# Performance work log

Measured on AMD Instinct MI355X. Metric: run time of the kernel, lower is better.

The kernel has to match this reference:

```python
import jax, jax.numpy as jnp
import numpy as np
from jax import lax

# pywt 'db6' rec_lo (scaling filter). dec_lo = rec_lo[::-1]; pytorch_wavelets
# stores dec filters flipped for conv (=correlation), so analysis correlation
# filters are exactly rec_lo and rec_hi = qmf(rec_lo). Synthesis filters for
# conv_transpose are rec_lo/rec_hi unflipped -> same arrays.
_DB6 = np.array([0.11154074335008017, 0.4946238903983854, 0.7511339080215775,
                 0.3152503517092432, -0.22626469396516913, -0.12976686756709563,
                 0.09750160558707936, 0.02752286553001629, -0.031582039318031156,
                 0.0005538422009938016, 0.004777257511010651, -0.00107730108499558],
                dtype=np.float32)
_QMF = (_DB6[::-1].copy() * ((-1.0) ** np.arange(12))).astype(np.float32)
H0, H1 = jnp.asarray(_DB6), jnp.asarray(_QMF)
LF, J = 12, 3
BATCH, SEQ_LEN, CH = 128, 720, 321
COMP_L = [99, 365, 188, 99]   # [yl, yh1, yh2, yh3] for seq_len=720
OUT_L = [22, 57, 34, 22]      # same decomposition of red_len=104


def afb1d(x):
    """One-level analysis filter bank, mode='symmetric'. x: [B,C,N]."""
    B, C, N = x.shape
    out = (N + LF - 1) // 2                      # pywt dwt_coeff_len (symmetric)
    p = 2 * (out - 1) - N + LF
    xp = jnp.pad(x, ((0, 0), (0, 0), (p // 2, (p + 1) // 2)), mode='symmetric')
    w = jnp.stack([H0, H1])[:, None, :]          # [2,1,LF]
    y = lax.conv_general_dilated(xp.reshape(B * C, 1, -1), w, (2,), 'VALID',
                                 dimension_numbers=('NCH', 'OIH', 'NCH'))
    y = y.reshape(B, C, 2, out)
    return y[:, :, 0], y[:, :, 1]


def sfb1d(lo, hi):
    """One-level synthesis bank == conv_transpose1d(stride=2, padding=LF-2)."""
    B, C, Lin = lo.shape
    z = jnp.stack([lo, hi], axis=2).reshape(B * C, 2, Lin)
    w = jnp.stack([H0[::-1], H1[::-1]])[None]    # [1,2,LF], flipped for corr
    y = lax.conv_general_dilated(z, w, (1,), ((1, 1),), lhs_dilation=(2,),
                                 dimension_numbers=('NCH', 'OIH', 'NCH'))
    return y.reshape(B, C, -1)                   # length 2*Lin + 2 - LF


def sinusoidal_pe(n_pos, d):
    pos = jnp.arange(n_pos, dtype=jnp.float32)[:, None]
    div = jnp.exp(jnp.arange(0, d, 2, dtype=jnp.float32) * (-np.log(10000.0) / d))
    pe = jnp.zeros((n_pos, d), jnp.float32)
    pe = pe.at[:, 0::2].set(jnp.sin(pos * div))
    pe = pe.at[:, 1::2].set(jnp.cos(pos * div[: d // 2]))
    return pe


def _forward(x, qws, qbs, kws, kbs, pws, pbs, iws, als, bes):
    mean = lax.stop_gradient(jnp.mean(x, axis=1, keepdims=True))
    std = lax.stop_gradient(jnp.sqrt(jnp.var(x, axis=1, keepdims=True) + 1e-5))
    xc = jnp.transpose((x - mean) / std, (0, 2, 1))      # [B,C,L]
    yl, yh = xc, []
    for _ in range(J):
        yl, hi = afb1d(yl)
        yh.append(hi)
    decomps = [yl] + yh                                  # lengths COMP_L
    preds = []
    for i, comp in enumerate(decomps):
        B, C, L = comp.shape
        Q = jnp.tanh(comp @ qws[i].T + qbs[i])           # [B,C,L]
        K = jnp.tanh(comp @ kws[i].T + kbs[i])
        scores = jnp.einsum('bcl,bcs->bls', Q, K) / (L ** 0.5)
        weighted = jnp.mean(jnp.tanh(scores), axis=1)    # [B,S] (equal per channel)
        cum = jnp.flip(jnp.cumsum(jnp.flip(weighted, -1), -1), -1)
        P = jax.nn.softmax(cum * als[i][0], axis=-1)
        idxs = jnp.arange(L, dtype=jnp.float32)
        win = jnp.sum(P * idxs, axis=-1)[:, None, None]  # soft truncation [B,1,1]
        mask = jax.nn.sigmoid((idxs[None, None, :] - win) * bes[i][0])
        pred = (comp * mask) @ pws[i].T + pbs[i]         # [B,C,O]
        pred = jax.nn.softmax(iws[i], axis=1) * (pred + sinusoidal_pe(C, pred.shape[-1])[None])
        preds.append(pred)
    ll = preds[0]
    for h in preds[:0:-1]:                               # coarsest high band first
        if ll.shape[-1] > h.shape[-1]:
            ll = ll[..., : h.shape[-1]]
        ll = sfb1d(ll, h)
    return ll, mean, std


def setup_inputs() -> dict:
    key = jax.random.key(0)
    ks = jax.random.split(key, 64)
    inp = {'x': jax.random.normal(ks[0], (BATCH, SEQ_LEN, CH), jnp.float32)}
    k = 1
    for i, (L, O) in enumerate(zip(COMP_L, OUT_L)):
        s = 1.0 / np.sqrt(L)                             # torch Linear default init
        inp[f'qw{i}'] = jax.random.uniform(ks[k], (L, L), jnp.float32, -s, s); k += 1
        inp[f'qb{i}'] = jax.random.uniform(ks[k], (L,), jnp.float32, -s, s); k += 1
        inp[f'kw{i}'] = jax.random.uniform(ks[k], (L, L), jnp.float32, -s, s); k += 1
        inp[f'kb{i}'] = jax.random.uniform(ks[k], (L,), jnp.float32, -s, s); k += 1
        inp[f'pw{i}'] = jnp.full((O, L), 1.0 / L, jnp.float32)
        inp[f'pb{i}'] = jnp.zeros((O,), jnp.float32)
        inp[f'iw{i}'] = jnp.ones((1, CH, O), jnp.float32)
        inp[f'al{i}'] = jnp.full((1,), 10.0, jnp.float32)
        inp[f'be{i}'] = jnp.full((1,), 10.0, jnp.float32)
    return inp


def reference(x, qw0, qb0, kw0, kb0, pw0, pb0, iw0, al0, be0,
              qw1, qb1, kw1, kb1, pw1, pb1, iw1, al1, be1,
              qw2, qb2, kw2, kb2, pw2, pb2, iw2, al2, be2,
              qw3, qb3, kw3, kb3, pw3, pb3, iw3, al3, be3):
    return _forward(x, [qw0, qw1, qw2, qw3], [qb0, qb1, qb2, qb3],
                    [kw0, kw1, kw2, kw3], [kb0, kb1, kb2, kb3],
                    [pw0, pw1, pw2, pw3], [pb0, pb1, pb2, pb3],
                    [iw0, iw1, iw2, iw3], [al0, al1, al2, al3],
                    [be0, be1, be2, be3])
```

## Files before the change

kernel.cpp:

```cpp
#include <hip/hip_runtime.h>
#include <hip/hip_bf16.h>
#include <math.h>

namespace {
constexpr int kB  = 128;
constexpr int kC  = 321;
constexpr int kN0 = 720;
constexpr int kCp = 384;
}

typedef __attribute__((ext_vector_type(8))) short short8;
typedef __attribute__((ext_vector_type(4))) float floatx4;

__constant__ float c_h0[12] = {
  0.11154074335008017f, 0.4946238903983854f, 0.7511339080215775f,
  0.3152503517092432f, -0.22626469396516913f, -0.12976686756709563f,
  0.09750160558707936f, 0.02752286553001629f, -0.031582039318031156f,
  0.0005538422009938016f, 0.004777257511010651f, -0.00107730108499558f};
__constant__ float c_h1[12] = {
  -0.00107730108499558f, -0.004777257511010651f, 0.0005538422009938016f,
  0.031582039318031156f, 0.02752286553001629f, -0.09750160558707936f,
  -0.12976686756709563f, 0.22626469396516913f, 0.3152503517092432f,
  -0.7511339080215775f, 0.4946238903983854f, -0.11154074335008017f};
__constant__ float c_h0r[12] = {
  -0.00107730108499558f, 0.004777257511010651f, 0.0005538422009938016f,
  -0.031582039318031156f, 0.02752286553001629f, 0.09750160558707936f,
  -0.12976686756709563f, -0.22626469396516913f, 0.3152503517092432f,
  0.7511339080215775f, 0.4946238903983854f, 0.11154074335008017f};
__constant__ float c_h1r[12] = {
  -0.11154074335008017f, 0.4946238903983854f, -0.7511339080215775f,
  0.3152503517092432f, 0.22626469396516913f, -0.12976686756709563f,
  -0.09750160558707936f, 0.02752286553001629f, 0.031582039318031156f,
  0.0005538422009938016f, -0.004777257511010651f, -0.00107730108499558f};

__device__ __forceinline__ float fast_tanh(float x) {
  float e = __expf(2.f * x);
  return 1.f - 2.f / (e + 1.f);
}
__device__ __forceinline__ unsigned short f2b(float f) {
  __hip_bfloat16 h = __float2bfloat16(f);
  return __builtin_bit_cast(unsigned short, h);
}

__device__ __forceinline__ void gload16(const unsigned short* g, short* l) {
  __builtin_amdgcn_global_load_lds(
      (const __attribute__((address_space(1))) unsigned int*)g,
      (__attribute__((address_space(3))) unsigned int*)l, 16, 0, 0);
}

__global__ void __launch_bounds__(128) partial_ms_kernel(
    const float* __restrict__ x, float* __restrict__ ps, float* __restrict__ ps2) {
  int b = blockIdx.x, chunk = blockIdx.y;
  int c = blockIdx.z * 128 + threadIdx.x;
  if (c >= kC) return;
  const float* xb = x + (size_t)b * kN0 * kC + c;
  int t0 = chunk * 90;
  float s = 0.f, s2 = 0.f;
#pragma unroll 15
  for (int i = 0; i < 90; ++i) {
    float v = xb[(size_t)(t0 + i) * kC];
    s += v; s2 += v * v;
  }
  ps [(b * 8 + chunk) * kC + c] = s;
  ps2[(b * 8 + chunk) * kC + c] = s2;
}

__global__ void __launch_bounds__(256) finalize_ms_kernel(
    const float* __restrict__ ps, const float* __restrict__ ps2,
    float* __restrict__ mout, float* __restrict__ sout,
    float* __restrict__ meanw, float* __restrict__ invw) {
  int i = blockIdx.x * 256 + threadIdx.x;
  if (i >= kB * kC) return;
  int b = i / kC, c = i - b * kC;
  float s = 0.f, s2 = 0.f;
#pragma unroll
  for (int k = 0; k < 8; ++k) { s += ps[(b * 8 + k) * kC + c]; s2 += ps2[(b * 8 + k) * kC + c]; }
  float mean = s * (1.f / (float)kN0);
  float var = s2 * (1.f / (float)kN0) - mean * mean;
  float sd = sqrtf(var + 1e-5f);
  mout[i] = mean; sout[i] = sd;
  meanw[i] = mean; invw[i] = 1.f / sd;
}

__device__ __forceinline__ int sym_reflect(int t, int N) {
  t = (t < 0) ? (-1 - t) : t;
  t = (t >= N) ? (2 * N - 1 - t) : t;
  return t;
}

template <bool NORM, bool LO_F32, bool LO_BF16>
__global__ void __launch_bounds__(256) dwt_fused_kernel(
    const float* __restrict__ in, const float* __restrict__ meanw,
    const float* __restrict__ invw, float* __restrict__ loF,
    unsigned short* __restrict__ loB, unsigned short* __restrict__ hiB,
    int N, int L, int Lp) {
  __shared__ float xs[138][64];
  __shared__ unsigned short los[64][72];
  __shared__ unsigned short his[64][72];
  const int b = blockIdx.z;
  const int n0 = blockIdx.x * 64, c0 = blockIdx.y * 64;
  const int tid = threadIdx.x;
  const int cl = tid & 63, wv = tid >> 6;
  const int c = c0 + cl;
  const int t0 = 2 * n0 - 10;
  const float* ib = in + (size_t)b * N * kC;
  float mean = 0.f, inv = 1.f;
  if (NORM && c < kC) { mean = meanw[b * kC + c]; inv = invw[b * kC + c]; }
  for (int r = wv; r < 138; r += 4) {
    int t = sym_reflect(t0 + r, N);
    float v = (c < kC) ? ib[(size_t)t * kC + c] : 0.f;
    if (NORM) v = (v - mean) * inv;
    xs[r][cl] = v;
  }
  __syncthreads();
#pragma unroll 4
  for (int k = 0; k < 16; ++k) {
    int nl = wv + 4 * k;
    int n = n0 + nl;
    float a0 = 0.f, a1 = 0.f;
    int base = 2 * nl;
#pragma unroll
    for (int j = 0; j < 12; ++j) {
      float v = xs[base + j][cl];
      a0 += v * c_h0[j]; a1 += v * c_h1[j];
    }
    bool valid = (n < L) && (c < kC);
    if (LO_F32 && valid) loF[((size_t)b * L + n) * kC + c] = a0;
    if (LO_BF16) los[cl][nl] = f2b(valid ? a0 : 0.f);
    his[cl][nl] = f2b(valid ? a1 : 0.f);
  }
  __syncthreads();
  int row = tid >> 2, part = tid & 3;
  size_t dst = ((size_t)b * kCp + c0 + row) * Lp + n0 + part * 16;
  *(uint4*)(hiB + dst)     = *(const uint4*)&his[row][part * 16];
  *(uint4*)(hiB + dst + 8) = *(const uint4*)&his[row][part * 16 + 8];
  if (LO_BF16) {
    *(uint4*)(loB + dst)     = *(const uint4*)&los[row][part * 16];
    *(uint4*)(loB + dst + 8) = *(const uint4*)&los[row][part * 16 + 8];
  }
}

struct WcArgs { const float* src[8]; unsigned short* dst[8]; int L[8]; int Lp[8]; };
__global__ void __launch_bounds__(256) wconv_all_kernel(WcArgs a) {
  int lvl = blockIdx.y;
  int Lp = a.Lp[lvl], L = a.L[lvl];
  int i = blockIdx.x * 256 + threadIdx.x;
  if (i >= Lp * Lp) return;
  int p = i / Lp, l = i - p * Lp;
  a.dst[lvl][i] = f2b((p < L && l < L) ? a.src[lvl][(size_t)p * L + l] : 0.f);
}

struct QKAllArgs {
  const unsigned short* W[8];
  const unsigned short* Xt[4];
  const float* bias[8];
  unsigned short* Y[8];
  int Lp[4], L[4], yOff[4];
};
__global__ void __launch_bounds__(256) qk_all_kernel(QKAllArgs a) {
  const int y = blockIdx.y;
  const int lvl = (y >= a.yOff[1]) + (y >= a.yOff[2]) + (y >= a.yOff[3]);
  const int Lp = a.Lp[lvl], L = a.L[lvl];
  const int pBase = (y - a.yOff[lvl]) * 128;
  const unsigned short* W0 = a.W[2 * lvl]     + (size_t)pBase * Lp;
  const unsigned short* W1 = a.W[2 * lvl + 1] + (size_t)pBase * Lp;
  const int b = blockIdx.z;
  const int cBase = blockIdx.x * 128;
  const int tid = threadIdx.x;
  const int ln = tid & 63, w = tid >> 6;
  const int wm = w & 1, wn = w >> 1;
  __shared__ short Aq[128 * 64];
  __shared__ short Ak[128 * 64];
  __shared__ short Bs[128 * 64];
  floatx4 acc[2][4][4] = {};
  const unsigned short* Xb = a.Xt[lvl] + ((size_t)b * kCp + cBase) * Lp;
  const int kIters = Lp >> 6;
  const int srow = w * 32;
  const int lrow = ln >> 3, lslot = ln & 7;
  const int gswz = (lslot ^ lrow) << 3;
  const int sc0 = (((ln >> 4) + 0) ^ (ln & 7)) << 3;
  const int sc1 = (((ln >> 4) + 4) ^ (ln & 7)) << 3;
  for (int kt = 0; kt < kIters; ++kt) {
    const int lc = kt << 6;
#pragma unroll
    for (int q = 0; q < 4; ++q) {
      const int row = srow + 8 * q + lrow;
      const size_t goff = (size_t)row * Lp + lc + gswz;
      short* ldst = (short*)&Aq[(srow + 8 * q) * 64];
      gload16(W0 + goff, ldst);
      gload16(W1 + goff, ldst + 128 * 64);
      gload16(Xb + goff, ldst + 2 * 128 * 64);
    }
    __syncthreads();
#pragma unroll
    for (int sub = 0; sub < 2; ++sub) {
      const int sc = sub ? sc1 : sc0;
      short8 a0[4], a1[4], bv[4];
#pragma unroll
      for (int mi = 0; mi < 4; ++mi) {
        const int ar = (wm * 64 + mi * 16 + (ln & 15)) * 64 + sc;
        a0[mi] = *(const short8*)&Aq[ar];
        a1[mi] = *(const short8*)&Ak[ar];
      }
#pragma unroll
      for (int ni = 0; ni < 4; ++ni)
        bv[ni] = *(const short8*)&Bs[(wn * 64 + ni * 16 + (ln & 15)) * 64 + sc];
#pragma unroll
      for (int mi = 0; mi < 4; ++mi)
#pragma unroll
        for (int ni = 0; ni < 4; ++ni) {
          acc[0][mi][ni] = __builtin_amdgcn_mfma_f32_16x16x32_bf16(a0[mi], bv[ni], acc[0][mi][ni], 0, 0, 0);
          acc[1][mi][ni] = __builtin_amdgcn_mfma_f32_16x16x32_bf16(a1[mi], bv[ni], acc[1][mi][ni], 0, 0, 0);
        }
    }
    __syncthreads();
  }
#pragma unroll
  for (int s = 0; s < 2; ++s) {
    const float* bias = a.bias[2 * lvl + s];
    unsigned short* Yd = a.Y[2 * lvl + s];
#pragma unroll
    for (int mi = 0; mi < 4; ++mi) {
#pragma unroll
      for (int r = 0; r < 4; ++r) {
        int p = pBase + wm * 64 + mi * 16 + (ln >> 4) * 4 + r;
        float bv = (p < L) ? bias[p] : 0.f;
#pragma unroll
        for (int ni = 0; ni < 4; ++ni) {
          int c = cBase + wn * 64 + ni * 16 + (ln & 15);
          float v = (p < L && c < kC) ? fast_tanh(acc[s][mi][ni][r] + bv) : 0.f;
          Yd[((size_t)b * Lp + p) * kCp + c] = f2b(v);
        }
      }
    }
  }
}

struct ScAllArgs {
  const unsigned short* Q[4]; const unsigned short* K[4];
  float* wgt[4];
  int Lp[4], L[4], tOff[4];
  float scale[4];
};
__global__ void __launch_bounds__(256) scores_all_kernel(ScAllArgs a) {
  const int t = blockIdx.x;
  const int lvl = (t >= a.tOff[1]) + (t >= a.tOff[2]) + (t >= a.tOff[3]);
  const int rel = t - a.tOff[lvl];
  const int Lp = a.Lp[lvl], L = a.L[lvl];
  const int pt = Lp >> 7;
  const int sBase = (rel % pt) * 128;
  const int lBase = (rel / pt) * 128;
  const int b = blockIdx.y;
  const int tid = threadIdx.x;
  const int ln = tid & 63, w = tid >> 6;
  const int wm = w & 1, wn = w >> 1;
  __shared__ short As[128 * 64];
  __shared__ short Bs[128 * 64];
  __shared__ float red[128];
  floatx4 acc[4][4] = {};
  const unsigned short* Qp = a.Q[lvl] + ((size_t)b * Lp + lBase) * kCp;
  const unsigned short* Kp = a.K[lvl] + ((size_t)b * Lp + sBase) * kCp;
  const int srow = w * 32;
  const int lrow = ln >> 3, lslot = ln & 7;
  const int gswz = (lslot ^ lrow) << 3;
  const int sc0 = (((ln >> 4) + 0) ^ (ln & 7)) << 3;
  const int sc1 = (((ln >> 4) + 4) ^ (ln & 7)) << 3;
  for (int cc = 0; cc < kCp; cc += 64) {
#pragma unroll
    for (int q = 0; q < 4; ++q) {
      const int row = srow + 8 * q + lrow;
      const size_t goff = (size_t)row * kCp + cc + gswz;
      short* ldst = (short*)&As[(srow + 8 * q) * 64];
      gload16(Qp + goff, ldst);
      gload16(Kp + goff, ldst + 128 * 64);
    }
    __syncthreads();
#pragma unroll
    for (int sub = 0; sub < 2; ++sub) {
      const int sc = sub ? sc1 : sc0;
      short8 av[4], bv[4];
#pragma unroll
      for (int mi = 0; mi < 4; ++mi)
        av[mi] = *(const short8*)&As[(wm * 64 + mi * 16 + (ln & 15)) * 64 + sc];
#pragma unroll
      for (int ni = 0; ni < 4; ++ni)
        bv[ni] = *(const short8*)&Bs[(wn * 64 + ni * 16 + (ln & 15)) * 64 + sc];
#pragma unroll
      for (int mi = 0; mi < 4; ++mi)
#pragma unroll
        for (int ni = 0; ni < 4; ++ni)
          acc[mi][ni] = __builtin_amdgcn_mfma_f32_16x16x32_bf16(av[mi], bv[ni], acc[mi][ni], 0, 0, 0);
    }
    __syncthreads();
  }
  if (tid < 128) red[tid] = 0.f;
  __syncthreads();
  const float scale = a.scale[lvl];
#pragma unroll
  for (int ni = 0; ni < 4; ++ni) {
    float p = 0.f;
#pragma unroll
    for (int mi = 0; mi < 4; ++mi)
#pragma unroll
      for (int r = 0; r < 4; ++r) p += fast_tanh(acc[mi][ni][r] * scale);
    p += __shfl_xor(p, 16);
    p += __shfl_xor(p, 32);
    if ((ln & 48) == 0) atomicAdd(&red[wn * 64 + ni * 16 + (ln & 15)], p);
  }
  __syncthreads();
  if (tid < 128) {
    int s = sBase + tid;
    if (s < L) atomicAdd(&a.wgt[lvl][(size_t)b * L + s], red[tid]);
  }
}

struct WinArgs { const float* wgt[4]; const float* al[4]; const float* be[4];
                 float* mask[4]; int L[4]; };
__global__ void __launch_bounds__(64) winmask_all_kernel(WinArgs a) {
  int lvl = blockIdx.y;
  int b = blockIdx.x, lane = threadIdx.x;
  int L = a.L[lvl];
  const float* wgt = a.wgt[lvl] + (size_t)b * L;
  float al = a.al[lvl][0], be = a.be[lvl][0];
  float invL = 1.f / (float)L;
  int chunk = (L + 63) >> 6;
  int s0 = lane * chunk;
  float v[6];
  float csum = 0.f;
  for (int i = chunk - 1; i >= 0; --i) {
    int s = s0 + i;
    float xv = (s < L) ? wgt[s] * invL : 0.f;
    csum += xv; v[i] = csum;
  }
  float tot = csum;
  for (int o = 1; o < 64; o <<= 1) {
    float t = __shfl_down(tot, o);
    if (lane + o < 64) tot += t;
  }
  float excl = tot - csum;
  float m = -1e30f;
  for (int i = 0; i < chunk; ++i)
    if (s0 + i < L) m = fmaxf(m, al * (v[i] + excl));
  for (int o = 32; o; o >>= 1) m = fmaxf(m, __shfl_xor(m, o));
  float sum = 0.f, num = 0.f;
  for (int i = 0; i < chunk; ++i) {
    int s = s0 + i;
    if (s < L) { float e = __expf(al * (v[i] + excl) - m); sum += e; num += e * (float)s; }
  }
  for (int o = 32; o; o >>= 1) { sum += __shfl_xor(sum, o); num += __shfl_xor(num, o); }
  float win = num / sum;
  float* mk = a.mask[lvl] + (size_t)b * L;
  for (int i = 0; i < chunk; ++i) {
    int s = s0 + i;
    if (s < L) mk[s] = 1.f / (1.f + __expf(-((float)s - win) * be));
  }
}

struct IwArgs { const float* iw[4]; float* sm[4]; int O[4]; };
__global__ void __launch_bounds__(64) iwsm_all_kernel(IwArgs a) {
  int x = blockIdx.x;
  int lvl, o;
  if (x < 22) { lvl = 0; o = x; }
  else if (x < 79) { lvl = 1; o = x - 22; }
  else if (x < 113) { lvl = 2; o = x - 79; }
  else { lvl = 3; o = x - 113; }
  int O = a.O[lvl];
  const float* iw = a.iw[lvl];
  int lane = threadIdx.x;
  float m = -1e30f;
  for (int c = lane; c < kC; c += 64) m = fmaxf(m, iw[c * O + o]);
  for (int k = 32; k; k >>= 1) m = fmaxf(m, __shfl_xor(m, k));
  float sum = 0.f;
  for (int c = lane; c < kC; c += 64) sum += __expf(iw[c * O + o] - m);
  for (int k = 32; k; k >>= 1) sum += __shfl_xor(sum, k);
  float inv = 1.f / sum;
  for (int c = lane; c < kC; c += 64) a.sm[lvl][c * O + o] = __expf(iw[c * O + o] - m) * inv;
}

struct PredAllArgs {
  const unsigned short* Xt[4];
  const float* PW[4]; const float* PB[4]; const float* MK[4]; const float* SM[4];
  float* OUT[4];
  int L[4], Lp[4], O[4];
};
__global__ void __launch_bounds__(256) pred_all_kernel(PredAllArgs a) {
  const int lvl = blockIdx.y;
  const int L = a.L[lvl], Lp = a.Lp[lvl], O = a.O[lvl];
  const float* PW = a.PW[lvl];
  const int b = blockIdx.z;
  const int cBase = blockIdx.x * 128;
  const int tid = threadIdx.x;
  const int ln = tid & 63, w = tid >> 6;
  __shared__ short As[64 * 40];
  __shared__ short Bs[128 * 40];
  floatx4 acc[8] = {};
  const unsigned short* Xb = a.Xt[lvl] + ((size_t)b * kCp + cBase) * Lp;
  const float* mk = a.MK[lvl] + (size_t)b * L;
  for (int lc = 0; lc < Lp; lc += 32) {
    {
      int o = tid >> 2, j0 = (tid & 3) * 8;
      alignas(16) unsigned short tmp[8];
#pragma unroll
      for (int j = 0; j < 8; ++j) {
        int l = lc + j0 + j;
        float v = (o < O && l < L) ? PW[(size_t)o * L + l] * mk[l] : 0.f;
        tmp[j] = f2b(v);
      }
      *(uint4*)&As[o * 40 + j0] = *(const uint4*)tmp;
    }
#pragma unroll
    for (int q = 0; q < 2; ++q) {
      int ch = tid * 2 + q;
      int row = ch >> 2, pos = ch & 3;
      *(uint4*)(&Bs[row * 40 + pos * 8]) = *(const uint4*)(Xb + (size_t)row * Lp + lc + pos * 8);
    }
    __syncthreads();
    short8 av = *(const short8*)&As[(w * 16 + (ln & 15)) * 40 + (ln >> 4) * 8];
#pragma unroll
    for (int ni = 0; ni < 8; ++ni) {
      short8 bb = *(const short8*)&Bs[(ni * 16 + (ln & 15)) * 40 + (ln >> 4) * 8];
      acc[ni] = __builtin_amdgcn_mfma_f32_16x16x32_bf16(av, bb, acc[ni], 0, 0, 0);
    }
    __syncthreads();
  }
  const float negln = -logf(10000.f) / (float)O;
#pragma unroll
  for (int ni = 0; ni < 8; ++ni) {
    int c = cBase + ni * 16 + (ln & 15);
    if (c >= kC) continue;
#pragma unroll
    for (int r = 0; r < 4; ++r) {
      int o = w * 16 + (ln >> 4) * 4 + r;
      if (o >= O) continue;
      float dv = __expf(negln * (float)(2 * (o >> 1)));
      float ang = (float)c * dv;
      float pe = (o & 1) ? cosf(ang) : sinf(ang);
      a.OUT[lvl][((size_t)b * O + o) * kC + c] = a.SM[lvl][c * O + o] * (acc[ni][r] + a.PB[lvl][o] + pe);
    }
  }
}

__global__ void __launch_bounds__(256) sfb_fused_kernel(
    const float* __restrict__ P0, const float* __restrict__ P1,
    const float* __restrict__ P2, const float* __restrict__ P3,
    float* __restrict__ out) {
  __shared__ float p0s[22][32], p3s[22][32], p2s[34][32], p1s[57][32];
  __shared__ float r1s[34][32], r2s[58][32];
  __shared__ float outs[104][33];
  int b = blockIdx.y, c0 = blockIdx.x * 32;
  int tid = threadIdx.x;
  int cl = tid & 31, r = tid >> 5;
  int c = c0 + cl;
  bool cv = c < kC;
  for (int o = r; o < 22; o += 8) {
    p0s[o][cl] = cv ? P0[((size_t)b * 22 + o) * kC + c] : 0.f;
    p3s[o][cl] = cv ? P3[((size_t)b * 22 + o) * kC + c] : 0.f;
  }
  for (int o = r; o < 34; o += 8) p2s[o][cl] = cv ? P2[((size_t)b * 34 + o) * kC + c] : 0.f;
  for (int o = r; o < 57; o += 8) p1s[o][cl] = cv ? P1[((size_t)b * 57 + o) * kC + c] : 0.f;
  __syncthreads();
  for (int n = r; n < 34; n += 8) {
    float acc = 0.f;
#pragma unroll
    for (int j = 0; j < 12; ++j) {
      int m = n + j - 1;
      if (m < 0 || (m & 1)) continue;
      int i = m >> 1;
      if (i >= 22) continue;
      acc += c_h0r[j] * p0s[i][cl] + c_h1r[j] * p3s[i][cl];
    }
    r1s[n][cl] = acc;
  }
  __syncthreads();
  for (int n = r; n < 58; n += 8) {
    float acc = 0.f;
#pragma unroll
    for (int j = 0; j < 12; ++j) {
      int m = n + j - 1;
      if (m < 0 || (m & 1)) continue;
      int i = m >> 1;
      if (i >= 34) continue;
      acc += c_h0r[j] * r1s[i][cl] + c_h1r[j] * p2s[i][cl];
    }
    r2s[n][cl] = acc;
  }
  __syncthreads();
  for (int n = r; n < 104; n += 8) {
    float acc = 0.f;
#pragma unroll
    for (int j = 0; j < 12; ++j) {
      int m = n + j - 1;
      if (m < 0 || (m & 1)) continue;
      int i = m >> 1;
      if (i >= 57) continue;
      acc += c_h0r[j] * r2s[i][cl] + c_h1r[j] * p1s[i][cl];
    }
    outs[n][cl] = acc;
  }
  __syncthreads();
  for (int idx = tid; idx < 32 * 104; idx += 256) {
    int ci = idx / 104, n = idx - ci * 104;
    int cg = c0 + ci;
    if (cg < kC) out[((size_t)b * kC + cg) * 104 + n] = outs[n][ci];
  }
}

extern "C" void kernel_launch(void* const* d_in, const int* in_sizes, int n_in,
                              void* d_out, int out_size, void* d_ws, size_t ws_size,
                              hipStream_t stream) {
  (void)in_sizes; (void)n_in; (void)out_size; (void)ws_size;
  const float* x = (const float*)d_in[0];
  auto inp = [&](int lvl, int j) { return (const float*)d_in[1 + 9 * lvl + j]; };

  float* outf = (float*)d_out;
  float* mout = outf + (size_t)kB * kC * 104;
  float* sout = mout + (size_t)kB * kC;

  float* Wp = (float*)d_ws;
  size_t off = 0;
  auto alloc = [&](size_t n) { float* p = Wp + off; off += (n + 63) & ~(size_t)63; return p; };

  float* LO1 = alloc((size_t)kB * 365 * kC);
  float* LO2 = alloc((size_t)kB * 188 * kC);
  unsigned short* Xt1 = (unsigned short*)alloc((size_t)kB * kCp * 384 / 2);
  unsigned short* Xt2 = (unsigned short*)alloc((size_t)kB * kCp * 256 / 2);
  unsigned short* Xt0 = (unsigned short*)alloc((size_t)kB * kCp * 128 / 2);
  unsigned short* Xt3 = (unsigned short*)alloc((size_t)kB * kCp * 128 / 2);
  unsigned short* KbfAll = (unsigned short*)alloc((size_t)kB * kCp * 896 / 2);
  unsigned short* Wpv[8];
  for (int i = 0; i < 8; ++i)
    Wpv[i] = (unsigned short*)alloc((size_t)384 * 384 / 2);
  float* wgtAll = alloc((size_t)kB * (99 + 365 + 188 + 99));
  float* M0 = alloc((size_t)kB * 99);  float* M1 = alloc((size_t)kB * 365);
  float* M2 = alloc((size_t)kB * 188); float* M3 = alloc((size_t)kB * 99);
  float* S0 = alloc((size_t)kC * 22);  float* S1 = alloc((size_t)kC * 57);
  float* S2 = alloc((size_t)kC * 34);  float* S3 = alloc((size_t)kC * 22);
  float* P0 = alloc((size_t)kB * 22 * kC); float* P1 = alloc((size_t)kB * 57 * kC);
  float* P2 = alloc((size_t)kB * 34 * kC); float* P3 = alloc((size_t)kB * 22 * kC);
  float* ps   = alloc((size_t)kB * 8 * kC);
  float* ps2  = alloc((size_t)kB * 8 * kC);
  float* meanw = alloc((size_t)kB * kC);
  float* invw  = alloc((size_t)kB * kC);
  unsigned short* QbfAll = (unsigned short*)LO1;

  const int Lc[4]  = {99, 365, 188, 99};
  const int Lpv[4] = {128, 384, 256, 128};
  const int Ov[4]  = {22, 57, 34, 22};
  const int prefLp[4] = {0, 128, 512, 768};
  const int wOff[4] = {0, 99, 99 + 365, 99 + 365 + 188};
  unsigned short* Qlvl[4]; unsigned short* Klvl[4];
  for (int i = 0; i < 4; ++i) {
    Qlvl[i] = QbfAll + (size_t)kB * kCp * prefLp[i];
    Klvl[i] = KbfAll + (size_t)kB * kCp * prefLp[i];
  }
  const unsigned short* Xts[4] = {Xt0, Xt1, Xt2, Xt3};
  float* masks[4] = {M0, M1, M2, M3};
  float* smws[4]  = {S0, S1, S2, S3};
  float* preds[4] = {P0, P1, P2, P3};

  partial_ms_kernel<<<dim3(kB, 8, 3), 128, 0, stream>>>(x, ps, ps2);
  finalize_ms_kernel<<<(kB * kC + 255) / 256, 256, 0, stream>>>(ps, ps2, mout, sout, meanw, invw);

  dwt_fused_kernel<true, true, false><<<dim3(6, kCp / 64, kB), 256, 0, stream>>>(
      x, meanw, invw, LO1, nullptr, Xt1, kN0, 365, 384);
  dwt_fused_kernel<false, true, false><<<dim3(4, kCp / 64, kB), 256, 0, stream>>>(
      LO1, nullptr, nullptr, LO2, nullptr, Xt2, 365, 188, 256);
  dwt_fused_kernel<false, false, true><<<dim3(2, kCp / 64, kB), 256, 0, stream>>>(
      LO2, nullptr, nullptr, nullptr, Xt0, Xt3, 188, 99, 128);

  {
    WcArgs wa;
    for (int i = 0; i < 4; ++i) {
      wa.src[2 * i] = inp(i, 0); wa.src[2 * i + 1] = inp(i, 2);
      wa.dst[2 * i] = Wpv[2 * i]; wa.dst[2 * i + 1] = Wpv[2 * i + 1];
      wa.L[2 * i] = wa.L[2 * i + 1] = Lc[i];
      wa.Lp[2 * i] = wa.Lp[2 * i + 1] = Lpv[i];
    }
    wconv_all_kernel<<<dim3(576, 8), 256, 0, stream>>>(wa);
  }
  hipMemsetAsync(wgtAll, 0, (size_t)kB * (99 + 365 + 188 + 99) * sizeof(float), stream);

  {
    QKAllArgs qa;
    for (int i = 0; i < 4; ++i) {
      qa.W[2 * i] = Wpv[2 * i]; qa.W[2 * i + 1] = Wpv[2 * i + 1];
      qa.bias[2 * i] = inp(i, 1); qa.bias[2 * i + 1] = inp(i, 3);
      qa.Y[2 * i] = Qlvl[i]; qa.Y[2 * i + 1] = Klvl[i];
      qa.Xt[i] = Xts[i]; qa.Lp[i] = Lpv[i]; qa.L[i] = Lc[i];
    }
    qa.yOff[0] = 0; qa.yOff[1] = 1; qa.yOff[2] = 4; qa.yOff[3] = 6;
    qk_all_kernel<<<dim3(kCp / 128, 7, kB), 256, 0, stream>>>(qa);
  }

  {
    ScAllArgs sa;
    for (int i = 0; i < 4; ++i) {
      sa.Q[i] = Qlvl[i]; sa.K[i] = Klvl[i];
      sa.wgt[i] = wgtAll + (size_t)kB * wOff[i];
      sa.Lp[i] = Lpv[i]; sa.L[i] = Lc[i];
      sa.scale[i] = 1.0f / sqrtf((float)Lc[i]);
    }
    sa.tOff[0] = 0; sa.tOff[1] = 1; sa.tOff[2] = 10; sa.tOff[3] = 14;
    scores_all_kernel<<<dim3(15, kB), 256, 0, stream>>>(sa);
  }

  {
    WinArgs wa;
    for (int i = 0; i < 4; ++i) {
      wa.wgt[i] = wgtAll + (size_t)kB * wOff[i];
      wa.al[i] = inp(i, 7); wa.be[i] = inp(i, 8);
      wa.mask[i] = masks[i]; wa.L[i] = Lc[i];
    }
    winmask_all_kernel<<<dim3(kB, 4), 64, 0, stream>>>(wa);
    IwArgs ia;
    for (int i = 0; i < 4; ++i) { ia.iw[i] = inp(i, 6); ia.sm[i] = smws[i]; ia.O[i] = Ov[i]; }
    iwsm_all_kernel<<<135, 64, 0, stream>>>(ia);
  }

  {
    PredAllArgs pa;
    for (int i = 0; i < 4; ++i) {
      pa.Xt[i] = Xts[i]; pa.PW[i] = inp(i, 4); pa.PB[i] = inp(i, 5);
      pa.MK[i] = masks[i]; pa.SM[i] = smws[i]; pa.OUT[i] = preds[i];
      pa.L[i] = Lc[i]; pa.Lp[i] = Lpv[i]; pa.O[i] = Ov[i];
    }
    pred_all_kernel<<<dim3(kCp / 128, 4, kB), 256, 0, stream>>>(pa);
  }

  sfb_fused_kernel<<<dim3(11, kB), 256, 0, stream>>>(P0, P1, P2, P3, outf);
}
```

Before: 865.4 us.

## Double-buffer LDS and retile QK and scores GEMMs with 512-thread blocks

Both the QK projection and the scores GEMM kernels now use 8 waves per block with a double-buffered shared-memory pipeline, so the next K-tile's global loads are issued while the current tile is being multiplied. The QK kernel narrows its column tile from 128 to 64, which doubles the grid, and gives each wave a 16-row strip. The scores kernel splits work 4x2 across waves. The aim is to hide global load latency and raise occupancy. The cost is more shared memory per block and re-reading the W tiles across more column blocks. The QK epilogue also simplifies its masking so that each output applies only one bound check.

```diff
diff --git a/kernel.cpp b/kernel.cpp
--- a/kernel.cpp
+++ b/kernel.cpp
@@ -157,7 +157,7 @@
   unsigned short* Y[8];
   int Lp[4], L[4], yOff[4];
 };
-__global__ void __launch_bounds__(256) qk_all_kernel(QKAllArgs a) {
+__global__ void __launch_bounds__(512, 4) qk_all_kernel(QKAllArgs a) {
   const int y = blockIdx.y;
   const int lvl = (y >= a.yOff[1]) + (y >= a.yOff[2]) + (y >= a.yOff[3]);
   const int Lp = a.Lp[lvl], L = a.L[lvl];
@@ -165,53 +165,51 @@
   const unsigned short* W0 = a.W[2 * lvl]     + (size_t)pBase * Lp;
   const unsigned short* W1 = a.W[2 * lvl + 1] + (size_t)pBase * Lp;
   const int b = blockIdx.z;
-  const int cBase = blockIdx.x * 128;
+  const int cBase = blockIdx.x * 64;
   const int tid = threadIdx.x;
   const int ln = tid & 63, w = tid >> 6;
-  const int wm = w & 1, wn = w >> 1;
-  __shared__ short Aq[128 * 64];
-  __shared__ short Ak[128 * 64];
-  __shared__ short Bs[128 * 64];
-  floatx4 acc[2][4][4] = {};
+  __shared__ short smem[2 * 320 * 64];
+  floatx4 acc[2][4] = {};
   const unsigned short* Xb = a.Xt[lvl] + ((size_t)b * kCp + cBase) * Lp;
-  const int kIters = Lp >> 6;
-  const int srow = w * 32;
-  const int lrow = ln >> 3, lslot = ln & 7;
-  const int gswz = (lslot ^ lrow) << 3;
-  const int sc0 = (((ln >> 4) + 0) ^ (ln & 7)) << 3;
-  const int sc1 = (((ln >> 4) + 4) ^ (ln & 7)) << 3;
-  for (int kt = 0; kt < kIters; ++kt) {
-    const int lc = kt << 6;
-#pragma unroll
-    for (int q = 0; q < 4; ++q) {
-      const int row = srow + 8 * q + lrow;
-      const size_t goff = (size_t)row * Lp + lc + gswz;
-      short* ldst = (short*)&Aq[(srow + 8 * q) * 64];
-      gload16(W0 + goff, ldst);
-      gload16(W1 + goff, ldst + 128 * 64);
-      gload16(Xb + goff, ldst + 2 * 128 * 64);
-    }
-    __syncthreads();
+  const int lrow = ln >> 3;
+  const int gswz = ((ln & 7) ^ lrow) << 3;
+  const unsigned short* srcs[5];
+#pragma unroll
+  for (int i = 0; i < 5; ++i) {
+    int o = w * 5 + i;
+    int rr = o * 8 + lrow;
+    const unsigned short* s = (o < 16) ? (W0 + (size_t)rr * Lp)
+                            : (o < 32) ? (W1 + (size_t)(rr - 128) * Lp)
+                                       : (Xb + (size_t)(rr - 256) * Lp);
+    srcs[i] = s + gswz;
+  }
+  const int nt = Lp >> 6;
+#pragma unroll
+  for (int i = 0; i < 5; ++i) gload16(srcs[i], &smem[(w * 5 + i) * 512]);
+  __syncthreads();
+  for (int kt = 0; kt < nt; ++kt) {
+    const int ph = (kt & 1) * 20480;
+    if (kt + 1 < nt) {
+      const int phn = ((kt + 1) & 1) * 20480;
+      const int lc = (kt + 1) << 6;
+#pragma unroll
+      for (int i = 0; i < 5; ++i) gload16(srcs[i] + lc, &smem[phn + (w * 5 + i) * 512]);
+    }
 #pragma unroll
     for (int sub = 0; sub < 2; ++sub) {
-      const int sc = sub ? sc1 : sc0;
-      short8 a0[4], a1[4], bv[4];
-#pragma unroll
-      for (int mi = 0; mi < 4; ++mi) {
-        const int ar = (wm * 64 + mi * 16 + (ln & 15)) * 64 + sc;
-        a0[mi] = *(const short8*)&Aq[ar];
-        a1[mi] = *(const short8*)&Ak[ar];
+      const int sc = (((ln >> 4) + sub * 4) ^ (ln & 7)) << 3;
+      const int ar = (w * 16 + (ln & 15)) * 64 + sc;
+      short8 aq = *(const short8*)&smem[ph + ar];
+      short8 ak = *(const short8*)&smem[ph + 8192 + ar];
+      short8 bv[4];
+#pragma unroll
+      for (int ni = 0; ni < 4; ++ni)
+        bv[ni] = *(const short8*)&smem[ph + 16384 + (ni * 16 + (ln & 15)) * 64 + sc];
+#pragma unroll
+      for (int ni = 0; ni < 4; ++ni) {
+        acc[0][ni] = __builtin_amdgcn_mfma_f32_16x16x32_bf16(aq, bv[ni], acc[0][ni], 0, 0, 0);
+        acc[1][ni] = __builtin_amdgcn_mfma_f32_16x16x32_bf16(ak, bv[ni], acc[1][ni], 0, 0, 0);
       }
-#pragma unroll
-      for (int ni = 0; ni < 4; ++ni)
-        bv[ni] = *(const short8*)&Bs[(wn * 64 + ni * 16 + (ln & 15)) * 64 + sc];
-#pragma unroll
-      for (int mi = 0; mi < 4; ++mi)
-#pragma unroll
-        for (int ni = 0; ni < 4; ++ni) {
-          acc[0][mi][ni] = __builtin_amdgcn_mfma_f32_16x16x32_bf16(a0[mi], bv[ni], acc[0][mi][ni], 0, 0, 0);
-          acc[1][mi][ni] = __builtin_amdgcn_mfma_f32_16x16x32_bf16(a1[mi], bv[ni], acc[1][mi][ni], 0, 0, 0);
-        }
     }
     __syncthreads();
   }
@@ -220,17 +218,17 @@
     const float* bias = a.bias[2 * lvl + s];
     unsigned short* Yd = a.Y[2 * lvl + s];
 #pragma unroll
-    for (int mi = 0; mi < 4; ++mi) {
-#pragma unroll
-      for (int r = 0; r < 4; ++r) {
-        int p = pBase + wm * 64 + mi * 16 + (ln >> 4) * 4 + r;
-        float bv = (p < L) ? bias[p] : 0.f;
-#pragma unroll
-        for (int ni = 0; ni < 4; ++ni) {
-          int c = cBase + wn * 64 + ni * 16 + (ln & 15);
-          float v = (p < L && c < kC) ? fast_tanh(acc[s][mi][ni][r] + bv) : 0.f;
-          Yd[((size_t)b * Lp + p) * kCp + c] = f2b(v);
-        }
+    for (int r = 0; r < 4; ++r) {
+      int p = pBase + w * 16 + (ln >> 4) * 4 + r;
+      bool pv = (p < L);
+      float bvf = pv ? bias[p] : 0.f;
+#pragma unroll
+      for (int ni = 0; ni < 4; ++ni) {
+        int c = cBase + ni * 16 + (ln & 15);
+        float v = fast_tanh(acc[s][ni][r] + bvf);
+        if (s == 0) { if (!pv) v = 0.f; }
+        else        { if (c >= kC) v = 0.f; }
+        Yd[((size_t)b * Lp + p) * kCp + c] = f2b(v);
       }
     }
   }
@@ -242,7 +240,7 @@
   int Lp[4], L[4], tOff[4];
   float scale[4];
 };
-__global__ void __launch_bounds__(256) scores_all_kernel(ScAllArgs a) {
+__global__ void __launch_bounds__(512, 4) scores_all_kernel(ScAllArgs a) {
   const int t = blockIdx.x;
   const int lvl = (t >= a.tOff[1]) + (t >= a.tOff[2]) + (t >= a.tOff[3]);
   const int rel = t - a.tOff[lvl];
@@ -253,54 +251,59 @@
   const int b = blockIdx.y;
   const int tid = threadIdx.x;
   const int ln = tid & 63, w = tid >> 6;
-  const int wm = w & 1, wn = w >> 1;
-  __shared__ short As[128 * 64];
-  __shared__ short Bs[128 * 64];
+  const int wm = w & 3, wn = w >> 2;
+  __shared__ short smem[2 * 256 * 64];
   __shared__ float red[128];
-  floatx4 acc[4][4] = {};
+  floatx4 acc[2][4] = {};
   const unsigned short* Qp = a.Q[lvl] + ((size_t)b * Lp + lBase) * kCp;
   const unsigned short* Kp = a.K[lvl] + ((size_t)b * Lp + sBase) * kCp;
-  const int srow = w * 32;
-  const int lrow = ln >> 3, lslot = ln & 7;
-  const int gswz = (lslot ^ lrow) << 3;
-  const int sc0 = (((ln >> 4) + 0) ^ (ln & 7)) << 3;
-  const int sc1 = (((ln >> 4) + 4) ^ (ln & 7)) << 3;
-  for (int cc = 0; cc < kCp; cc += 64) {
-#pragma unroll
-    for (int q = 0; q < 4; ++q) {
-      const int row = srow + 8 * q + lrow;
-      const size_t goff = (size_t)row * kCp + cc + gswz;
-      short* ldst = (short*)&As[(srow + 8 * q) * 64];
-      gload16(Qp + goff, ldst);
-      gload16(Kp + goff, ldst + 128 * 64);
-    }
-    __syncthreads();
+  const int lrow = ln >> 3;
+  const int gswz = ((ln & 7) ^ lrow) << 3;
+  const unsigned short* srcs[4];
+#pragma unroll
+  for (int i = 0; i < 4; ++i) {
+    int o = w * 4 + i;
+    int rr = o * 8 + lrow;
+    srcs[i] = ((o < 16) ? (Qp + (size_t)rr * kCp)
+                        : (Kp + (size_t)(rr - 128) * kCp)) + gswz;
+  }
+#pragma unroll
+  for (int i = 0; i < 4; ++i) gload16(srcs[i], &smem[(w * 4 + i) * 512]);
+  if (tid < 128) red[tid] = 0.f;
+  __syncthreads();
+  const int nt = kCp >> 6;
+  for (int kt = 0; kt < nt; ++kt) {
+    const int ph = (kt & 1) * 16384;
+    if (kt + 1 < nt) {
+      const int phn = ((kt + 1) & 1) * 16384;
+      const int cc = (kt + 1) << 6;
+#pragma unroll
+      for (int i = 0; i < 4; ++i) gload16(srcs[i] + cc, &smem[phn + (w * 4 + i) * 512]);
+    }
 #pragma unroll
     for (int sub = 0; sub < 2; ++sub) {
-      const int sc = sub ? sc1 : sc0;
-      short8 av[4], bv[4];
-#pragma unroll
-      for (int mi = 0; mi < 4; ++mi)
-        av[mi] = *(const short8*)&As[(wm * 64 + mi * 16 + (ln & 15)) * 64 + sc];
+      const int sc = (((ln >> 4) + sub * 4) ^ (ln & 7)) << 3;
+      short8 av[2], bv[4];
+#pragma unroll
+      for (int mi = 0; mi < 2; ++mi)
+        av[mi] = *(const short8*)&smem[ph + (wm * 32 + mi * 16 + (ln & 15)) * 64 + sc];
 #pragma unroll
       for (int ni = 0; ni < 4; ++ni)
-        bv[ni] = *(const short8*)&Bs[(wn * 64 + ni * 16 + (ln & 15)) * 64 + sc];
-#pragma unroll
-      for (int mi = 0; mi < 4; ++mi)
+        bv[ni] = *(const short8*)&smem[ph + 8192 + (wn * 64 + ni * 16 + (ln & 15)) * 64 + sc];
+#pragma unroll
+      for (int mi = 0; mi < 2; ++mi)
 #pragma unroll
         for (int ni = 0; ni < 4; ++ni)
           acc[mi][ni] = __builtin_amdgcn_mfma_f32_16x16x32_bf16(av[mi], bv[ni], acc[mi][ni], 0, 0, 0);
     }
     __syncthreads();
   }
-  if (tid < 128) red[tid] = 0.f;
-  __syncthreads();
   const float scale = a.scale[lvl];
 #pragma unroll
   for (int ni = 0; ni < 4; ++ni) {
     float p = 0.f;
 #pragma unroll
-    for (int mi = 0; mi < 4; ++mi)
+    for (int mi = 0; mi < 2; ++mi)
 #pragma unroll
       for (int r = 0; r < 4; ++r) p += fast_tanh(acc[mi][ni][r] * scale);
     p += __shfl_xor(p, 16);
@@ -589,7 +592,7 @@
       qa.Xt[i] = Xts[i]; qa.Lp[i] = Lpv[i]; qa.L[i] = Lc[i];
     }
     qa.yOff[0] = 0; qa.yOff[1] = 1; qa.yOff[2] = 4; qa.yOff[3] = 6;
-    qk_all_kernel<<<dim3(kCp / 128, 7, kB), 256, 0, stream>>>(qa);
+    qk_all_kernel<<<dim3(kCp / 64, 7, kB), 512, 0, stream>>>(qa);
   }
 
   {
@@ -601,7 +604,7 @@
       sa.scale[i] = 1.0f / sqrtf((float)Lc[i]);
     }
     sa.tOff[0] = 0; sa.tOff[1] = 1; sa.tOff[2] = 10; sa.tOff[3] = 14;
-    scores_all_kernel<<<dim3(15, kB), 256, 0, stream>>>(sa);
+    scores_all_kernel<<<dim3(15, kB), 512, 0, stream>>>(sa);
   }
 
   {
```

Result: faster. 808.2 us (-6.6%).
